# Kernel tuning notes

Measured on AMD Instinct MI355X. Metric: run time of the kernel, lower is better.

The kernel has to match this reference:

```python
import jax, jax.numpy as jnp
import numpy as np

K = 7          # kernel_size
PAD = 3        # padding (same-size output)
GROUPS = 8


def _unfold(z, H, W):
    # z: [B, C, H+2p, W+2p] -> patches [B, C, H, W, K*K], flat index = kh*K + kw
    # matches torch .unfold(2,K,1).unfold(3,K,1).view(..., -1)
    return jnp.stack(
        [z[:, :, a:a + H, b:b + W] for a in range(K) for b in range(K)],
        axis=-1,
    )


def setup_inputs() -> dict:
    key = jax.random.key(0)
    ks = jax.random.split(key, 7)
    B, C, H, W = 4, 64, 64, 64
    Cout = 64
    fan_scale = (2.0 / Cout) ** 0.5  # kaiming fan_out, 1x1 conv
    return {
        "x": jax.random.normal(ks[0], (B, C, H, W), jnp.float32),
        "y": jax.random.normal(ks[1], (B, C, H, W), jnp.float32),
        "Wq": jax.random.normal(ks[2], (Cout, C), jnp.float32) * fan_scale,
        "Wk": jax.random.normal(ks[3], (Cout, C), jnp.float32) * fan_scale,
        "Wv": jax.random.normal(ks[4], (Cout, C), jnp.float32) * fan_scale,
        "rel_h": jax.random.normal(ks[5], (Cout // 2, K), jnp.float32),
        "rel_w": jax.random.normal(ks[6], (Cout // 2, K), jnp.float32),
    }


def reference(x, y, Wq, Wk, Wv, rel_h, rel_w):
    B, C, H, W = x.shape
    Cout = Wq.shape[0]
    half = Cout // 2

    # 1x1 convs (no bias) commute with zero padding, so project first.
    q = jnp.einsum('oc,bchw->bohw', Wq, x)          # [B, Cout, H, W]
    k_full = jnp.einsum('oc,bchw->bohw', Wk, x)
    v_full = jnp.einsum('oc,bchw->bohw', Wv, y)

    pad4 = ((0, 0), (0, 0), (PAD, PAD), (PAD, PAD))
    k_pat = _unfold(jnp.pad(k_full, pad4), H, W)    # [B, Cout, H, W, K*K]
    v_pat = _unfold(jnp.pad(v_full, pad4), H, W)

    # relative-position bias: rel_h over kh (top half of channels), rel_w over kw
    bias_h = jnp.broadcast_to(rel_h[:, :, None], (half, K, K))   # [Cout/2, kh, kw]
    bias_w = jnp.broadcast_to(rel_w[:, None, :], (half, K, K))
    bias = jnp.concatenate([bias_h, bias_w], axis=0).reshape(Cout, K * K)
    k_pat = k_pat + bias[None, :, None, None, :]

    cg = Cout // GROUPS
    k_pat = k_pat.reshape(B, GROUPS, cg, H, W, K * K)
    v_pat = v_pat.reshape(B, GROUPS, cg, H, W, K * K)
    q = q.reshape(B, GROUPS, cg, H, W, 1)

    attn = jax.nn.softmax(q * k_pat, axis=-1)       # per-channel softmax over window
    out = jnp.sum(attn * v_pat, axis=-1)            # [B, G, cg, H, W]
    return out.reshape(B, Cout, H, W)
```

## Files before the change

kernel.cpp:

```cpp
#include <hip/hip_runtime.h>

#define HW 4096

typedef float f4 __attribute__((ext_vector_type(4)));

__global__ __launch_bounds__(64) void proj_kernel(
    const float* __restrict__ x, const float* __restrict__ y,
    const float* __restrict__ Wq, const float* __restrict__ Wk,
    const float* __restrict__ Wv,
    float* __restrict__ qkv)
{
    const int blk = blockIdx.x;
    const int pc  = blk & 255;
    const int sp  = blk >> 8;
    const int m   = sp >> 2;
    const int cb  = (sp & 3) << 4;
    const int px  = pc * 64 + threadIdx.x;
    const int b   = px >> 12;
    const int pp  = px & 4095;

    const float* W   = (m == 0) ? Wq : (m == 1) ? Wk : Wv;
    const float* src = (m == 2) ? y : x;
    const float* sb  = src + (size_t)b * 64 * HW + pp;

    float xv[64];
#pragma unroll
    for (int c = 0; c < 64; ++c)
        xv[c] = sb[c * HW];

    float* dstm = qkv + (size_t)m * (1 << 20) + (size_t)b * 64 * HW + pp;
#pragma unroll
    for (int i = 0; i < 16; ++i) {
        const float* wr = W + (cb + i) * 64;
        float acc = 0.f;
#pragma unroll
        for (int c = 0; c < 64; ++c)
            acc = fmaf(wr[c], xv[c], acc);
        dstm[(size_t)(cb + i) * HW] = acc;
    }
}

__global__ __launch_bounds__(256) void attn_kernel(
    const float* __restrict__ qg, const float* __restrict__ kg,
    const float* __restrict__ vg,
    const float* __restrict__ rel_h, const float* __restrict__ rel_w,
    float* __restrict__ out)
{
    __shared__ float kT[22 * 72];
    __shared__ float vT[22 * 72];

    const int blk = blockIdx.x;
    const int bc  = blk >> 2;
    const int h0  = (blk & 3) << 4;
    const int c   = bc & 63;
    const int t   = threadIdx.x;

    const float* kimg = kg + (size_t)bc * HW;
    const float* vimg = vg + (size_t)bc * HW;
    const f4 z4 = {0.f, 0.f, 0.f, 0.f};

    if (t < 88) {
        const int row = t >> 2, side = (t >> 1) & 1, arr = t & 1;
        float* dst = arr ? vT : kT;
        *(f4*)&dst[row * 72 + side * 68] = z4;
    }
#pragma unroll
    for (int j = 0; j < 2; ++j) {
        const int idx = j * 256 + t;
        if (idx < 352) {
            const int row = idx >> 4, ch = idx & 15;
            const int hy = h0 - 3 + row;
            const bool rv = ((unsigned)hy < 64u);
            const f4 kv = rv ? *(const f4*)&kimg[hy * 64 + ch * 4] : z4;
            const f4 vv = rv ? *(const f4*)&vimg[hy * 64 + ch * 4] : z4;
            *(f4*)&kT[row * 72 + ch * 4 + 4] = kv;
            *(f4*)&vT[row * 72 + ch * 4 + 4] = vv;
        }
    }
    __syncthreads();

    const int r  = t >> 4;
    const int w0 = (t & 15) << 2;
    const int h  = h0 + r;

    const float LOG2E = 1.4426950408889634f;
    const f4 qv = *(const f4*)&qg[(size_t)bc * HW + h * 64 + w0];
    float qe[4];
#pragma unroll
    for (int p = 0; p < 4; ++p) qe[p] = qv[p] * LOG2E;

    float qb[7][4];
    if (c < 32) {
#pragma unroll
        for (int a = 0; a < 7; ++a) {
            const float bb = rel_h[c * 7 + a];
#pragma unroll
            for (int p = 0; p < 4; ++p) qb[a][p] = qe[p] * bb;
        }
    } else {
#pragma unroll
        for (int j = 0; j < 7; ++j) {
            const float bb = rel_w[(c - 32) * 7 + j];
#pragma unroll
            for (int p = 0; p < 4; ++p) qb[j][p] = qe[p] * bb;
        }
    }

    float l[4] = {0.f, 0.f, 0.f, 0.f};
    float o[4] = {0.f, 0.f, 0.f, 0.f};

    if (c < 32) {
#pragma unroll
        for (int a = 0; a < 7; ++a) {
            const int ro = (r + a) * 72 + w0;
            const f4 k0 = *(const f4*)&kT[ro];
            const f4 k1 = *(const f4*)&kT[ro + 4];
            const f4 k2 = *(const f4*)&kT[ro + 8];
            const f4 v0 = *(const f4*)&vT[ro];
            const f4 v1 = *(const f4*)&vT[ro + 4];
            const f4 v2 = *(const f4*)&vT[ro + 8];
            const float kw[12] = {k0[0], k0[1], k0[2], k0[3], k1[0], k1[1], k1[2], k1[3],
                                  k2[0], k2[1], k2[2], k2[3]};
            const float vw[12] = {v0[0], v0[1], v0[2], v0[3], v1[0], v1[1], v1[2], v1[3],
                                  v2[0], v2[1], v2[2], v2[3]};
#pragma unroll
            for (int b2 = 0; b2 < 7; ++b2)
#pragma unroll
                for (int p = 0; p < 4; ++p) {
                    const float s = fmaf(qe[p], kw[p + b2 + 1], qb[a][p]);
                    const float e = __builtin_amdgcn_exp2f(s);
                    l[p] += e;
                    o[p] = fmaf(e, vw[p + b2 + 1], o[p]);
                }
        }
    } else {
#pragma unroll
        for (int a = 0; a < 7; ++a) {
            const int ro = (r + a) * 72 + w0;
            const f4 k0 = *(const f4*)&kT[ro];
            const f4 k1 = *(const f4*)&kT[ro + 4];
            const f4 k2 = *(const f4*)&kT[ro + 8];
            const f4 v0 = *(const f4*)&vT[ro];
            const f4 v1 = *(const f4*)&vT[ro + 4];
            const f4 v2 = *(const f4*)&vT[ro + 8];
            const float kw[12] = {k0[0], k0[1], k0[2], k0[3], k1[0], k1[1], k1[2], k1[3],
                                  k2[0], k2[1], k2[2], k2[3]};
            const float vw[12] = {v0[0], v0[1], v0[2], v0[3], v1[0], v1[1], v1[2], v1[3],
                                  v2[0], v2[1], v2[2], v2[3]};
#pragma unroll
            for (int b2 = 0; b2 < 7; ++b2)
#pragma unroll
                for (int p = 0; p < 4; ++p) {
                    const float s = fmaf(qe[p], kw[p + b2 + 1], qb[b2][p]);
                    const float e = __builtin_amdgcn_exp2f(s);
                    l[p] += e;
                    o[p] = fmaf(e, vw[p + b2 + 1], o[p]);
                }
        }
    }

    f4 res;
#pragma unroll
    for (int p = 0; p < 4; ++p)
        res[p] = o[p] * __builtin_amdgcn_rcpf(l[p]);
    *(f4*)&out[(size_t)bc * HW + h * 64 + w0] = res;
}

extern "C" void kernel_launch(void* const* d_in, const int* in_sizes, int n_in,
                              void* d_out, int out_size, void* d_ws, size_t ws_size,
                              hipStream_t stream) {
    const float* x   = (const float*)d_in[0];
    const float* y   = (const float*)d_in[1];
    const float* Wq  = (const float*)d_in[2];
    const float* Wk  = (const float*)d_in[3];
    const float* Wv  = (const float*)d_in[4];
    const float* rlh = (const float*)d_in[5];
    const float* rlw = (const float*)d_in[6];
    float* out = (float*)d_out;

    float* qkv = (float*)d_ws;
    float* q = qkv;
    float* k = qkv + (1 << 20);
    float* v = qkv + (2 << 20);

    proj_kernel<<<3072, 64, 0, stream>>>(x, y, Wq, Wk, Wv, qkv);
    attn_kernel<<<1024, 256, 0, stream>>>(q, k, v, rlh, rlw, out);
}
```

Baseline: 104.2 us.

## Fuse projection and attention into one persistent kernel with grid barrier

Merges the 1x1 projection and windowed attention kernels into a single launch of 512 blocks. Each wave computes 24 projected rows per pixel instead of 16, and a software grid barrier (atomic counter plus release flag) separates the two phases. Blocks then loop over two attention tiles each. This removes one kernel launch and the gap between the kernels, at the cost of a memset, a spin barrier that relies on all 512 blocks being co-resident, and reduced parallelism in the attention phase.

```diff
diff --git a/kernel.cpp b/kernel.cpp
--- a/kernel.cpp
+++ b/kernel.cpp
@@ -4,166 +4,193 @@
 
 typedef float f4 __attribute__((ext_vector_type(4)));
 
-__global__ __launch_bounds__(64) void proj_kernel(
+__global__ __launch_bounds__(256, 4) void fused_kernel(
     const float* __restrict__ x, const float* __restrict__ y,
     const float* __restrict__ Wq, const float* __restrict__ Wk,
     const float* __restrict__ Wv,
-    float* __restrict__ qkv)
-{
-    const int blk = blockIdx.x;
-    const int pc  = blk & 255;
-    const int sp  = blk >> 8;
-    const int m   = sp >> 2;
-    const int cb  = (sp & 3) << 4;
-    const int px  = pc * 64 + threadIdx.x;
-    const int b   = px >> 12;
-    const int pp  = px & 4095;
-
-    const float* W   = (m == 0) ? Wq : (m == 1) ? Wk : Wv;
-    const float* src = (m == 2) ? y : x;
-    const float* sb  = src + (size_t)b * 64 * HW + pp;
-
-    float xv[64];
-#pragma unroll
-    for (int c = 0; c < 64; ++c)
-        xv[c] = sb[c * HW];
-
-    float* dstm = qkv + (size_t)m * (1 << 20) + (size_t)b * 64 * HW + pp;
-#pragma unroll
-    for (int i = 0; i < 16; ++i) {
-        const float* wr = W + (cb + i) * 64;
-        float acc = 0.f;
-#pragma unroll
-        for (int c = 0; c < 64; ++c)
-            acc = fmaf(wr[c], xv[c], acc);
-        dstm[(size_t)(cb + i) * HW] = acc;
-    }
-}
-
-__global__ __launch_bounds__(256) void attn_kernel(
-    const float* __restrict__ qg, const float* __restrict__ kg,
-    const float* __restrict__ vg,
     const float* __restrict__ rel_h, const float* __restrict__ rel_w,
+    float* __restrict__ qkv,
+    unsigned* __restrict__ bar,
     float* __restrict__ out)
 {
     __shared__ float kT[22 * 72];
     __shared__ float vT[22 * 72];
 
-    const int blk = blockIdx.x;
-    const int bc  = blk >> 2;
-    const int h0  = (blk & 3) << 4;
-    const int c   = bc & 63;
-    const int t   = threadIdx.x;
-
-    const float* kimg = kg + (size_t)bc * HW;
-    const float* vimg = vg + (size_t)bc * HW;
-    const f4 z4 = {0.f, 0.f, 0.f, 0.f};
-
-    if (t < 88) {
-        const int row = t >> 2, side = (t >> 1) & 1, arr = t & 1;
-        float* dst = arr ? vT : kT;
-        *(f4*)&dst[row * 72 + side * 68] = z4;
+    const int t    = threadIdx.x;
+    const int lane = t & 63;
+    const int g    = blockIdx.x * 4 + (t >> 6);
+
+    {
+        const int sp = g >> 8;
+        const int r0 = sp * 24;
+        const int px = (g & 255) * 64 + lane;
+        const int b  = px >> 12;
+        const int pp = px & 4095;
+        const bool straddle = (r0 < 128) && (r0 + 24 > 128);
+
+        float iv[64];
+        {
+            const float* s0 = (r0 < 128) ? x : y;
+            const float* sb = s0 + (size_t)b * 64 * HW + pp;
+#pragma unroll
+            for (int c = 0; c < 64; ++c) iv[c] = sb[c * HW];
+        }
+
+#pragma unroll
+        for (int i = 0; i < 24; ++i) {
+            const int r = r0 + i;
+            if (straddle && r == 128) {
+                const float* sb = y + (size_t)b * 64 * HW + pp;
+#pragma unroll
+                for (int c = 0; c < 64; ++c) iv[c] = sb[c * HW];
+            }
+            const int m  = (r >= 64) + (r >= 128);
+            const float* wr = (r < 64)  ? Wq + r * 64
+                            : (r < 128) ? Wk + (r - 64) * 64
+                                        : Wv + (r - 128) * 64;
+            float acc = 0.f;
+#pragma unroll
+            for (int c = 0; c < 64; ++c)
+                acc = fmaf(wr[c], iv[c], acc);
+            qkv[(size_t)m * (1 << 20) + ((size_t)b * 64 + (r - m * 64)) * HW + pp] = acc;
+        }
     }
-#pragma unroll
-    for (int j = 0; j < 2; ++j) {
-        const int idx = j * 256 + t;
-        if (idx < 352) {
-            const int row = idx >> 4, ch = idx & 15;
-            const int hy = h0 - 3 + row;
-            const bool rv = ((unsigned)hy < 64u);
-            const f4 kv = rv ? *(const f4*)&kimg[hy * 64 + ch * 4] : z4;
-            const f4 vv = rv ? *(const f4*)&vimg[hy * 64 + ch * 4] : z4;
-            *(f4*)&kT[row * 72 + ch * 4 + 4] = kv;
-            *(f4*)&vT[row * 72 + ch * 4 + 4] = vv;
+
+    __syncthreads();
+    if (t == 0) {
+        __threadfence();
+        const unsigned old = atomicAdd(bar, 1u);
+        if (old == gridDim.x - 1) {
+            __hip_atomic_store(bar + 1, 1u, __ATOMIC_RELEASE, __HIP_MEMORY_SCOPE_AGENT);
+        } else {
+            while (__hip_atomic_load(bar + 1, __ATOMIC_ACQUIRE, __HIP_MEMORY_SCOPE_AGENT) == 0u)
+                __builtin_amdgcn_s_sleep(8);
         }
     }
     __syncthreads();
-
-    const int r  = t >> 4;
-    const int w0 = (t & 15) << 2;
-    const int h  = h0 + r;
-
+    __threadfence();
+
+    const float* qg = qkv;
+    const float* kg = qkv + (1 << 20);
+    const float* vg = qkv + (2 << 20);
+    const f4 z4 = {0.f, 0.f, 0.f, 0.f};
     const float LOG2E = 1.4426950408889634f;
-    const f4 qv = *(const f4*)&qg[(size_t)bc * HW + h * 64 + w0];
-    float qe[4];
-#pragma unroll
-    for (int p = 0; p < 4; ++p) qe[p] = qv[p] * LOG2E;
-
-    float qb[7][4];
-    if (c < 32) {
-#pragma unroll
-        for (int a = 0; a < 7; ++a) {
-            const float bb = rel_h[c * 7 + a];
-#pragma unroll
-            for (int p = 0; p < 4; ++p) qb[a][p] = qe[p] * bb;
-        }
-    } else {
-#pragma unroll
-        for (int j = 0; j < 7; ++j) {
-            const float bb = rel_w[(c - 32) * 7 + j];
-#pragma unroll
-            for (int p = 0; p < 4; ++p) qb[j][p] = qe[p] * bb;
-        }
+
+    for (int task = blockIdx.x; task < 1024; task += 512) {
+        __syncthreads();
+
+        const int bc = task >> 2;
+        const int h0 = (task & 3) << 4;
+        const int c  = bc & 63;
+
+        const float* kimg = kg + (size_t)bc * HW;
+        const float* vimg = vg + (size_t)bc * HW;
+
+        if (t < 88) {
+            const int row = t >> 2, side = (t >> 1) & 1, arr = t & 1;
+            float* dst = arr ? vT : kT;
+            *(f4*)&dst[row * 72 + side * 68] = z4;
+        }
+#pragma unroll
+        for (int j = 0; j < 2; ++j) {
+            const int idx = j * 256 + t;
+            if (idx < 352) {
+                const int row = idx >> 4, ch = idx & 15;
+                const int hy = h0 - 3 + row;
+                const bool rv = ((unsigned)hy < 64u);
+                const f4 kv = rv ? *(const f4*)&kimg[hy * 64 + ch * 4] : z4;
+                const f4 vv = rv ? *(const f4*)&vimg[hy * 64 + ch * 4] : z4;
+                *(f4*)&kT[row * 72 + ch * 4 + 4] = kv;
+                *(f4*)&vT[row * 72 + ch * 4 + 4] = vv;
+            }
+        }
+        __syncthreads();
+
+        const int r  = t >> 4;
+        const int w0 = (t & 15) << 2;
+        const int h  = h0 + r;
+
+        const f4 qv = *(const f4*)&qg[(size_t)bc * HW + h * 64 + w0];
+        float qe[4];
+#pragma unroll
+        for (int p = 0; p < 4; ++p) qe[p] = qv[p] * LOG2E;
+
+        float qb[7][4];
+        if (c < 32) {
+#pragma unroll
+            for (int a = 0; a < 7; ++a) {
+                const float bb = rel_h[c * 7 + a];
+#pragma unroll
+                for (int p = 0; p < 4; ++p) qb[a][p] = qe[p] * bb;
+            }
+        } else {
+#pragma unroll
+            for (int j = 0; j < 7; ++j) {
+                const float bb = rel_w[(c - 32) * 7 + j];
+#pragma unroll
+                for (int p = 0; p < 4; ++p) qb[j][p] = qe[p] * bb;
+            }
+        }
+
+        float l[4] = {0.f, 0.f, 0.f, 0.f};
+        float o[4] = {0.f, 0.f, 0.f, 0.f};
+
+        if (c < 32) {
+#pragma unroll
+            for (int a = 0; a < 7; ++a) {
+                const int ro = (r + a) * 72 + w0;
+                const f4 k0 = *(const f4*)&kT[ro];
+                const f4 k1 = *(const f4*)&kT[ro + 4];
+                const f4 k2 = *(const f4*)&kT[ro + 8];
+                const f4 v0 = *(const f4*)&vT[ro];
+                const f4 v1 = *(const f4*)&vT[ro + 4];
+                const f4 v2 = *(const f4*)&vT[ro + 8];
+                const float kw[12] = {k0[0], k0[1], k0[2], k0[3], k1[0], k1[1], k1[2], k1[3],
+                                      k2[0], k2[1], k2[2], k2[3]};
+                const float vw[12] = {v0[0], v0[1], v0[2], v0[3], v1[0], v1[1], v1[2], v1[3],
+                                      v2[0], v2[1], v2[2], v2[3]};
+#pragma unroll
+                for (int b2 = 0; b2 < 7; ++b2)
+#pragma unroll
+                    for (int p = 0; p < 4; ++p) {
+                        const float s = fmaf(qe[p], kw[p + b2 + 1], qb[a][p]);
+                        const float e = __builtin_amdgcn_exp2f(s);
+                        l[p] += e;
+                        o[p] = fmaf(e, vw[p + b2 + 1], o[p]);
+                    }
+            }
+        } else {
+#pragma unroll
+            for (int a = 0; a < 7; ++a) {
+                const int ro = (r + a) * 72 + w0;
+                const f4 k0 = *(const f4*)&kT[ro];
+                const f4 k1 = *(const f4*)&kT[ro + 4];
+                const f4 k2 = *(const f4*)&kT[ro + 8];
+                const f4 v0 = *(const f4*)&vT[ro];
+                const f4 v1 = *(const f4*)&vT[ro + 4];
+                const f4 v2 = *(const f4*)&vT[ro + 8];
+                const float kw[12] = {k0[0], k0[1], k0[2], k0[3], k1[0], k1[1], k1[2], k1[3],
+                                      k2[0], k2[1], k2[2], k2[3]};
+                const float vw[12] = {v0[0], v0[1], v0[2], v0[3], v1[0], v1[1], v1[2], v1[3],
+                                      v2[0], v2[1], v2[2], v2[3]};
+#pragma unroll
+                for (int b2 = 0; b2 < 7; ++b2)
+#pragma unroll
+                    for (int p = 0; p < 4; ++p) {
+                        const float s = fmaf(qe[p], kw[p + b2 + 1], qb[b2][p]);
+                        const float e = __builtin_amdgcn_exp2f(s);
+                        l[p] += e;
+                        o[p] = fmaf(e, vw[p + b2 + 1], o[p]);
+                    }
+            }
+        }
+
+        f4 res;
+#pragma unroll
+        for (int p = 0; p < 4; ++p)
+            res[p] = o[p] * __builtin_amdgcn_rcpf(l[p]);
+        *(f4*)&out[(size_t)bc * HW + h * 64 + w0] = res;
     }
-
-    float l[4] = {0.f, 0.f, 0.f, 0.f};
-    float o[4] = {0.f, 0.f, 0.f, 0.f};
-
-    if (c < 32) {
-#pragma unroll
-        for (int a = 0; a < 7; ++a) {
-            const int ro = (r + a) * 72 + w0;
-            const f4 k0 = *(const f4*)&kT[ro];
-            const f4 k1 = *(const f4*)&kT[ro + 4];
-            const f4 k2 = *(const f4*)&kT[ro + 8];
-            const f4 v0 = *(const f4*)&vT[ro];
-            const f4 v1 = *(const f4*)&vT[ro + 4];
-            const f4 v2 = *(const f4*)&vT[ro + 8];
-            const float kw[12] = {k0[0], k0[1], k0[2], k0[3], k1[0], k1[1], k1[2], k1[3],
-                                  k2[0], k2[1], k2[2], k2[3]};
-            const float vw[12] = {v0[0], v0[1], v0[2], v0[3], v1[0], v1[1], v1[2], v1[3],
-                                  v2[0], v2[1], v2[2], v2[3]};
-#pragma unroll
-            for (int b2 = 0; b2 < 7; ++b2)
-#pragma unroll
-                for (int p = 0; p < 4; ++p) {
-                    const float s = fmaf(qe[p], kw[p + b2 + 1], qb[a][p]);
-                    const float e = __builtin_amdgcn_exp2f(s);
-                    l[p] += e;
-                    o[p] = fmaf(e, vw[p + b2 + 1], o[p]);
-                }
-        }
-    } else {
-#pragma unroll
-        for (int a = 0; a < 7; ++a) {
-            const int ro = (r + a) * 72 + w0;
-            const f4 k0 = *(const f4*)&kT[ro];
-            const f4 k1 = *(const f4*)&kT[ro + 4];
-            const f4 k2 = *(const f4*)&kT[ro + 8];
-            const f4 v0 = *(const f4*)&vT[ro];
-            const f4 v1 = *(const f4*)&vT[ro + 4];
-            const f4 v2 = *(const f4*)&vT[ro + 8];
-            const float kw[12] = {k0[0], k0[1], k0[2], k0[3], k1[0], k1[1], k1[2], k1[3],
-                                  k2[0], k2[1], k2[2], k2[3]};
-            const float vw[12] = {v0[0], v0[1], v0[2], v0[3], v1[0], v1[1], v1[2], v1[3],
-                                  v2[0], v2[1], v2[2], v2[3]};
-#pragma unroll
-            for (int b2 = 0; b2 < 7; ++b2)
-#pragma unroll
-                for (int p = 0; p < 4; ++p) {
-                    const float s = fmaf(qe[p], kw[p + b2 + 1], qb[b2][p]);
-                    const float e = __builtin_amdgcn_exp2f(s);
-                    l[p] += e;
-                    o[p] = fmaf(e, vw[p + b2 + 1], o[p]);
-                }
-        }
-    }
-
-    f4 res;
-#pragma unroll
-    for (int p = 0; p < 4; ++p)
-        res[p] = o[p] * __builtin_amdgcn_rcpf(l[p]);
-    *(f4*)&out[(size_t)bc * HW + h * 64 + w0] = res;
 }
 
 extern "C" void kernel_launch(void* const* d_in, const int* in_sizes, int n_in,
@@ -178,11 +205,10 @@
     const float* rlw = (const float*)d_in[6];
     float* out = (float*)d_out;
 
-    float* qkv = (float*)d_ws;
-    float* q = qkv;
-    float* k = qkv + (1 << 20);
-    float* v = qkv + (2 << 20);
-
-    proj_kernel<<<3072, 64, 0, stream>>>(x, y, Wq, Wk, Wv, qkv);
-    attn_kernel<<<1024, 256, 0, stream>>>(q, k, v, rlh, rlw, out);
+    float*    qkv = (float*)d_ws;
+    unsigned* bar = (unsigned*)((char*)d_ws + (16u << 20));
+
+    hipMemsetAsync(bar, 0, 2 * sizeof(unsigned), stream);
+    fused_kernel<<<512, 256, 0, stream>>>(x, y, Wq, Wk, Wv, rlh, rlw,
+                                          qkv, bar, out);
 }
```

Measured after the change: 212.9 us. 104% more time.

## Stage projection input tile in LDS and compute 32 channels per thread

Applied to the files above, without the earlier changes.

The 1x1 projection kernel now loads a 64-channel by 256-pixel input tile into shared memory with vectorized loads, and each thread produces 32 output channels instead of 16. This reduces how many times each input pixel is re-read from global memory across channel splits and cuts the block count. In exchange it uses 64 KB of LDS per block and launches only 384 blocks, which can lower occupancy and balance across CUs.

```diff
diff --git a/kernel.cpp b/kernel.cpp
--- a/kernel.cpp
+++ b/kernel.cpp
@@ -4,39 +4,50 @@
 
 typedef float f4 __attribute__((ext_vector_type(4)));
 
-__global__ __launch_bounds__(64) void proj_kernel(
+__global__ __launch_bounds__(256) void proj_kernel(
     const float* __restrict__ x, const float* __restrict__ y,
     const float* __restrict__ Wq, const float* __restrict__ Wk,
     const float* __restrict__ Wv,
     float* __restrict__ qkv)
 {
-    const int blk = blockIdx.x;
-    const int pc  = blk & 255;
-    const int sp  = blk >> 8;
-    const int m   = sp >> 2;
-    const int cb  = (sp & 3) << 4;
-    const int px  = pc * 64 + threadIdx.x;
-    const int b   = px >> 12;
-    const int pp  = px & 4095;
+    __shared__ float xs[64 * 256];
+    const int t    = threadIdx.x;
+    const int fs   = blockIdx.x >> 6;
+    const int tile = blockIdx.x & 63;
+    const int fam  = fs >> 1;
+    const int r0   = (fs & 1) * 32;
+    const int b    = tile >> 4;
+    const int pp0  = (tile & 15) * 256;
 
-    const float* W   = (m == 0) ? Wq : (m == 1) ? Wk : Wv;
-    const float* src = (m == 2) ? y : x;
-    const float* sb  = src + (size_t)b * 64 * HW + pp;
+    const float* W   = (fam == 0) ? Wq : (fam == 1) ? Wk : Wv;
+    const float* src = (fam == 2) ? y : x;
+    const float* sb  = src + (size_t)b * 64 * HW + pp0;
 
+#pragma unroll
+    for (int s = 0; s < 16; ++s) {
+        const int fi  = s * 256 + t;
+        const int cin = fi >> 6, c4 = fi & 63;
+        const f4 v = *(const f4*)&sb[cin * HW + c4 * 4];
+        *(f4*)&xs[cin * 256 + c4 * 4] = v;
+    }
+    __syncthreads();
+
+    const int wv = t >> 6, lane = t & 63;
     float xv[64];
 #pragma unroll
     for (int c = 0; c < 64; ++c)
-        xv[c] = sb[c * HW];
+        xv[c] = xs[c * 256 + wv * 64 + lane];
 
-    float* dstm = qkv + (size_t)m * (1 << 20) + (size_t)b * 64 * HW + pp;
+    float* dst = qkv + ((size_t)fam << 20)
+                     + ((size_t)b * 64 + r0) * HW + pp0 + wv * 64 + lane;
 #pragma unroll
-    for (int i = 0; i < 16; ++i) {
-        const float* wr = W + (cb + i) * 64;
+    for (int j = 0; j < 32; ++j) {
+        const float* wr = W + (r0 + j) * 64;
         float acc = 0.f;
 #pragma unroll
         for (int c = 0; c < 64; ++c)
             acc = fmaf(wr[c], xv[c], acc);
-        dstm[(size_t)(cb + i) * HW] = acc;
+        dst[(size_t)j * HW] = acc;
     }
 }
 
@@ -61,8 +72,8 @@
 
     if (t < 88) {
         const int row = t >> 2, side = (t >> 1) & 1, arr = t & 1;
-        float* dst = arr ? vT : kT;
-        *(f4*)&dst[row * 72 + side * 68] = z4;
+        float* dstl = arr ? vT : kT;
+        *(f4*)&dstl[row * 72 + side * 68] = z4;
     }
 #pragma unroll
     for (int j = 0; j < 2; ++j) {
@@ -183,6 +194,6 @@
     float* k = qkv + (1 << 20);
     float* v = qkv + (2 << 20);
 
-    proj_kernel<<<3072, 64, 0, stream>>>(x, y, Wq, Wk, Wv, qkv);
+    proj_kernel<<<384, 256, 0, stream>>>(x, y, Wq, Wk, Wv, qkv);
     attn_kernel<<<1024, 256, 0, stream>>>(q, k, v, rlh, rlw, out);
 }
```

After: 120.8 us. 1.16x slower.
